# Kernel tuning notes

Measured on AMD Instinct MI355X. Metric: run time of the kernel, lower is better.

Reference implementation:

```python
import jax, jax.numpy as jnp
import numpy as np

B, L, D, DP = 64, 4096, 512, 64


def setup_inputs() -> dict:
    key = jax.random.key(0)
    ks = jax.random.split(key, 7)
    s = 0.02
    return {
        "source": jax.random.normal(ks[0], (B, D), jnp.float32),
        "main_embs": jax.random.normal(ks[1], (L, B, D), jnp.float32),   # time-major memory bank
        "pos_embs": jax.random.normal(ks[2], (L, B, DP), jnp.float32),
        "W_main_in": jax.random.normal(ks[3], (D, D), jnp.float32) * s,  # main_scorer.linear_in (no bias)
        "W_pos_in": jax.random.normal(ks[4], (D, DP), jnp.float32) * s,  # pos_scorer.linear_in (no bias)
        "W_out": jax.random.normal(ks[5], (D, 2 * D), jnp.float32) * s,  # linear_out (no bias, attn_type!='mlp')
        "memory_lengths": jnp.maximum(jax.random.randint(ks[6], (B,), 1, L + 1), 1),
    }


def reference(source, main_embs, pos_embs, W_main_in, W_pos_in, W_out, memory_lengths):
    # to batch-major: (B, L, D) / (B, L, DP)
    me = jnp.transpose(main_embs, (1, 0, 2))
    pe = jnp.transpose(pos_embs, (1, 0, 2))

    # 'general' scorer: project context then dot with query (qrs_len == 1)
    mc = jnp.einsum("bld,ed->ble", me, W_main_in)          # (B, L, D)
    main_align = jnp.einsum("bd,bld->bl", source, mc)      # (B, L)
    pc = jnp.einsum("blp,dp->bld", pe, W_pos_in)           # (B, L, D)
    pos_align = jnp.einsum("bd,bld->bl", source, pc)       # (B, L)

    # length mask + softmax on each branch
    mask = jnp.arange(me.shape[1])[None, :] < memory_lengths[:, None]  # (B, L)
    neg_inf = jnp.float32(-jnp.inf)
    ma = jax.nn.softmax(jnp.where(mask, main_align, neg_inf), axis=-1)
    pa = jax.nn.softmax(jnp.where(mask, pos_align, neg_inf), axis=-1)

    # elementwise combine + renormalize
    av = ma * pa
    av = av / jnp.sum(av, axis=-1, keepdims=True)

    # context vector + output projection + tanh
    c_t = jnp.einsum("bl,bld->bd", av, me)                 # (B, D)
    concat_c = jnp.concatenate([c_t, source], axis=-1)     # (B, 2D)
    attn_h = jnp.tanh(concat_c @ W_out.T)                  # (B, D)

    return attn_h, av, ma, pa
```

## Files before the change

kernel.cpp:

```cpp
#include <hip/hip_runtime.h>
#include <cstddef>

#define NB 64
#define NL 4096
#define ND 512
#define NDP 64
#define LC 64
#define NLC (NL / LC)

__global__ void __launch_bounds__(128) queries_kernel(
    const float* __restrict__ source, const float* __restrict__ Wmi,
    const float* __restrict__ Wpi, float* __restrict__ qpm,
    float* __restrict__ qpp)
{
    __shared__ float s[128];
    const int b  = blockIdx.x >> 2;
    const int eq = blockIdx.x & 3;
    const int t  = threadIdx.x;
    const int e0 = eq * 128;
    s[t] = source[b * ND + e0 + t];
    __syncthreads();

    const int d0 = t * 4;
    float4 a0 = {0,0,0,0}, a1 = {0,0,0,0};
    #pragma unroll 4
    for (int e = 0; e < 128; e += 2) {
        const float4 w0 = *(const float4*)(Wmi + (size_t)(e0 + e) * ND + d0);
        const float4 w1 = *(const float4*)(Wmi + (size_t)(e0 + e + 1) * ND + d0);
        const float x0 = s[e], x1 = s[e + 1];
        a0.x = fmaf(x0, w0.x, a0.x); a0.y = fmaf(x0, w0.y, a0.y);
        a0.z = fmaf(x0, w0.z, a0.z); a0.w = fmaf(x0, w0.w, a0.w);
        a1.x = fmaf(x1, w1.x, a1.x); a1.y = fmaf(x1, w1.y, a1.y);
        a1.z = fmaf(x1, w1.z, a1.z); a1.w = fmaf(x1, w1.w, a1.w);
    }
    a0.x += a1.x; a0.y += a1.y; a0.z += a1.z; a0.w += a1.w;
    *(float4*)(qpm + (size_t)(b * 4 + eq) * ND + d0) = a0;

    if (t < NDP) {
        float c0 = 0.f, c1 = 0.f;
        #pragma unroll 4
        for (int e = 0; e < 128; e += 2) {
            c0 = fmaf(s[e],     Wpi[(size_t)(e0 + e) * NDP + t],     c0);
            c1 = fmaf(s[e + 1], Wpi[(size_t)(e0 + e + 1) * NDP + t], c1);
        }
        qpp[(b * 4 + eq) * NDP + t] = c0 + c1;
    }
}

__global__ void __launch_bounds__(256) pass1_kernel(
    const float* __restrict__ me, const float* __restrict__ pe,
    const float* __restrict__ qpm, const float* __restrict__ qpp,
    const int* __restrict__ mem_len,
    float* __restrict__ a_main, float* __restrict__ a_pos,
    float* __restrict__ Sbuf, float* __restrict__ MZ,
    float* __restrict__ MZa, float* __restrict__ MZp)
{
    const int lane = threadIdx.x & 63;
    const int wid  = threadIdx.x >> 6;
    const int bg   = blockIdx.x & 15;
    const int lc   = blockIdx.x >> 4;
    const int b    = (((bg + (lc >> 4)) & 15) << 2) | wid;

    const int len = mem_len[b];
    const int l0  = lc * LC;
    if (l0 >= len) return;
    const int lend = min(l0 + LC, len);

    float4 q0 = {0,0,0,0}, q1 = {0,0,0,0};
    float qp = 0.f;
    #pragma unroll
    for (int eq = 0; eq < 4; ++eq) {
        const float4* qr = (const float4*)(qpm + (size_t)(b * 4 + eq) * ND);
        const float4 u0 = qr[lane], u1 = qr[64 + lane];
        q0.x += u0.x; q0.y += u0.y; q0.z += u0.z; q0.w += u0.w;
        q1.x += u1.x; q1.y += u1.y; q1.z += u1.z; q1.w += u1.w;
        qp += qpp[(b * 4 + eq) * NDP + lane];
    }

    float m = -1e30f, Z = 0.f;
    float Ma = -1e30f, Za = 0.f, Mp = -1e30f, Zp = 0.f;
    float4 S0 = {0,0,0,0}, S1 = {0,0,0,0};

    for (int l = l0; l < lend; ++l) {
        const size_t r = (size_t)l * NB + b;
        const float4* mrow = (const float4*)(me + r * ND);
        const float4 m0 = mrow[lane];
        const float4 m1 = mrow[64 + lane];

        float accm = m0.x*q0.x + m0.y*q0.y + m0.z*q0.z + m0.w*q0.w
                   + m1.x*q1.x + m1.y*q1.y + m1.z*q1.z + m1.w*q1.w;
        float accp = pe[r * NDP + lane] * qp;
        #pragma unroll
        for (int off = 32; off; off >>= 1) {
            accm += __shfl_xor(accm, off);
            accp += __shfl_xor(accp, off);
        }
        if (lane == 0) {
            a_main[(size_t)b * NL + l] = accm;
            a_pos [(size_t)b * NL + l] = accp;
        }

        const float sv = accm + accp;
        const float mn = fmaxf(m, sv);
        const float sc = __expf(m - mn);
        const float w  = __expf(sv - mn);
        Z = Z * sc + w;
        S0.x = fmaf(S0.x, sc, w * m0.x);  S0.y = fmaf(S0.y, sc, w * m0.y);
        S0.z = fmaf(S0.z, sc, w * m0.z);  S0.w = fmaf(S0.w, sc, w * m0.w);
        S1.x = fmaf(S1.x, sc, w * m1.x);  S1.y = fmaf(S1.y, sc, w * m1.y);
        S1.z = fmaf(S1.z, sc, w * m1.z);  S1.w = fmaf(S1.w, sc, w * m1.w);
        m = mn;

        const float mna = fmaxf(Ma, accm);
        Za = Za * __expf(Ma - mna) + __expf(accm - mna);
        Ma = mna;
        const float mnp = fmaxf(Mp, accp);
        Zp = Zp * __expf(Mp - mnp) + __expf(accp - mnp);
        Mp = mnp;
    }

    float* sp = Sbuf + ((size_t)b * NLC + lc) * ND;
    ((float4*)sp)[lane]      = S0;
    ((float4*)sp)[64 + lane] = S1;
    if (lane == 0) {
        const int idx = b * NLC + lc;
        MZ [2*idx] = m;  MZ [2*idx+1] = Z;
        MZa[2*idx] = Ma; MZa[2*idx+1] = Za;
        MZp[2*idx] = Mp; MZp[2*idx+1] = Zp;
    }
}

__global__ void __launch_bounds__(256) combineA_kernel(
    const float* __restrict__ MZ, const float* __restrict__ MZa,
    const float* __restrict__ MZp, const int* __restrict__ mem_len,
    float* __restrict__ coef, float* __restrict__ stats)
{
    const int lane = threadIdx.x & 63;
    const int b = blockIdx.x * 4 + (threadIdx.x >> 6);
    const int nv = (mem_len[b] + LC - 1) >> 6;
    const bool v = lane < nv;
    const int idx = b * NLC + lane;
    const float m  = v ? MZ [2*idx] : -1e30f;
    const float z  = v ? MZ [2*idx+1] : 0.f;
    const float ma = v ? MZa[2*idx] : -1e30f;
    const float za = v ? MZa[2*idx+1] : 0.f;
    const float mp = v ? MZp[2*idx] : -1e30f;
    const float zp = v ? MZp[2*idx+1] : 0.f;

    float M = m, A = ma, P = mp;
    #pragma unroll
    for (int off = 32; off; off >>= 1) {
        M = fmaxf(M, __shfl_xor(M, off));
        A = fmaxf(A, __shfl_xor(A, off));
        P = fmaxf(P, __shfl_xor(P, off));
    }
    float ez = z * __expf(m - M);
    float ea = za * __expf(ma - A);
    float ep = zp * __expf(mp - P);
    #pragma unroll
    for (int off = 32; off; off >>= 1) {
        ez += __shfl_xor(ez, off);
        ea += __shfl_xor(ea, off);
        ep += __shfl_xor(ep, off);
    }
    const float invZ = 1.f / ez;
    coef[idx] = v ? __expf(m - M) * invZ : 0.f;
    if (lane == 0) {
        stats[b*8+0] = A;  stats[b*8+1] = 1.f / ea;
        stats[b*8+2] = P;  stats[b*8+3] = 1.f / ep;
        stats[b*8+4] = M;  stats[b*8+5] = invZ;
    }
}

__global__ void __launch_bounds__(256) combineBF_kernel(
    const float* __restrict__ Sbuf, const float* __restrict__ coef,
    const float* __restrict__ stats, const int* __restrict__ mem_len,
    float* __restrict__ c_t,
    float* __restrict__ a_main, float* __restrict__ a_pos,
    float* __restrict__ out_av)
{
    if (blockIdx.x < 512) {
        __shared__ float sh[4][64];
        const int b = blockIdx.x >> 3, dseg = blockIdx.x & 7;
        const int dl = threadIdx.x & 63, k = threadIdx.x >> 6;
        const int d = dseg * 64 + dl;
        const int nv = (mem_len[b] + LC - 1) >> 6;
        float acc = 0.f;
        for (int lc = k; lc < nv; lc += 4)
            acc = fmaf(coef[b * NLC + lc],
                       Sbuf[((size_t)b * NLC + lc) * ND + d], acc);
        sh[k][dl] = acc;
        __syncthreads();
        if (threadIdx.x < 64)
            c_t[b * ND + dseg * 64 + threadIdx.x] =
                sh[0][threadIdx.x] + sh[1][threadIdx.x] +
                sh[2][threadIdx.x] + sh[3][threadIdx.x];
    } else {
        const int idx = (blockIdx.x - 512) * 256 + threadIdx.x;
        const int b = idx >> 12;
        const int l = idx & (NL - 1);
        const float* st = stats + b * 8;
        const int len = mem_len[b];
        const float a = a_main[idx];
        const float p = a_pos[idx];
        const bool v = l < len;
        a_main[idx] = v ? __expf(a - st[0]) * st[1] : 0.f;
        a_pos [idx] = v ? __expf(p - st[2]) * st[3] : 0.f;
        out_av[idx] = v ? __expf(a + p - st[4]) * st[5] : 0.f;
    }
}

__global__ void __launch_bounds__(256) out_kernel(
    const float* __restrict__ c_t, const float* __restrict__ source,
    const float* __restrict__ Wout, float* __restrict__ attn_h)
{
    __shared__ float cs[2 * ND];
    const int b = blockIdx.x >> 3;
    const int eg = blockIdx.x & 7;
    const int tid = threadIdx.x;

    for (int d = tid; d < ND; d += 256) {
        cs[d] = c_t[b * ND + d];
        cs[ND + d] = source[b * ND + d];
    }
    __syncthreads();

    const int wid = tid >> 6, lane = tid & 63;
    const float4* csv = (const float4*)cs;
    for (int e = eg * 64 + wid; e < eg * 64 + 64; e += 4) {
        const float4* wrow = (const float4*)(Wout + (size_t)e * 2 * ND);
        float acc = 0.f;
        #pragma unroll
        for (int j = 0; j < 4; ++j) {
            const float4 w = wrow[lane + 64 * j];
            const float4 c = csv[lane + 64 * j];
            acc += w.x * c.x + w.y * c.y + w.z * c.z + w.w * c.w;
        }
        #pragma unroll
        for (int off = 32; off; off >>= 1) acc += __shfl_xor(acc, off);
        if (lane == 0) attn_h[(size_t)b * ND + e] = tanhf(acc);
    }
}

extern "C" void kernel_launch(void* const* d_in, const int* in_sizes, int n_in,
                              void* d_out, int out_size, void* d_ws, size_t ws_size,
                              hipStream_t stream)
{
    const float* source = (const float*)d_in[0];
    const float* me     = (const float*)d_in[1];
    const float* pe     = (const float*)d_in[2];
    const float* Wmi    = (const float*)d_in[3];
    const float* Wpi    = (const float*)d_in[4];
    const float* Wout   = (const float*)d_in[5];
    const int*   lens   = (const int*)d_in[6];

    float* out    = (float*)d_out;
    float* attn_h = out;
    float* av     = attn_h + NB * ND;
    float* ma     = av + NB * NL;
    float* pa     = ma + NB * NL;

    float* ws    = (float*)d_ws;
    float* qpm   = ws;
    float* qpp   = qpm + NB * 4 * ND;
    float* Sbuf  = qpp + NB * 4 * NDP;
    float* MZ    = Sbuf + (size_t)NB * NLC * ND;
    float* MZa   = MZ  + NB * NLC * 2;
    float* MZp   = MZa + NB * NLC * 2;
    float* coef  = MZp + NB * NLC * 2;
    float* c_t   = coef + NB * NLC;
    float* stats = c_t + NB * ND;

    queries_kernel <<<NB * 4, 128, 0, stream>>>(source, Wmi, Wpi, qpm, qpp);
    pass1_kernel   <<<NLC * 16, 256, 0, stream>>>(me, pe, qpm, qpp, lens,
                                                  ma, pa, Sbuf, MZ, MZa, MZp);
    combineA_kernel<<<16, 256, 0, stream>>>(MZ, MZa, MZp, lens, coef, stats);
    combineBF_kernel<<<1536, 256, 0, stream>>>(Sbuf, coef, stats, lens,
                                               c_t, ma, pa, av);
    out_kernel     <<<NB * 8, 256, 0, stream>>>(c_t, source, Wout, attn_h);
}
```

Before: 119.7 us.

## Use persistent atomic work queue in pass1 with 4 waves per chunk

Pass1 becomes a persistent kernel of 1024 blocks that pull (chunk, batch) tasks from a global atomic counter. The four waves of a block now split the 64 rows of a single chunk, each taking every fourth row, instead of each wave handling a different batch row. Each wave also prefetches its next row while computing the current one, and partial softmax states are merged in shared memory before one write per chunk. The aim is to balance work across the skewed memory lengths and raise memory-level parallelism, at the cost of an extra memset, per-task atomics and block syncs.

```diff
diff --git a/kernel.cpp b/kernel.cpp
--- a/kernel.cpp
+++ b/kernel.cpp
@@ -7,6 +7,7 @@
 #define NDP 64
 #define LC 64
 #define NLC (NL / LC)
+#define NTASK (NB * NLC)
 
 __global__ void __launch_bounds__(128) queries_kernel(
     const float* __restrict__ source, const float* __restrict__ Wmi,
@@ -53,80 +54,141 @@
     const int* __restrict__ mem_len,
     float* __restrict__ a_main, float* __restrict__ a_pos,
     float* __restrict__ Sbuf, float* __restrict__ MZ,
-    float* __restrict__ MZa, float* __restrict__ MZp)
-{
-    const int lane = threadIdx.x & 63;
-    const int wid  = threadIdx.x >> 6;
-    const int bg   = blockIdx.x & 15;
-    const int lc   = blockIdx.x >> 4;
-    const int b    = (((bg + (lc >> 4)) & 15) << 2) | wid;
-
-    const int len = mem_len[b];
-    const int l0  = lc * LC;
-    if (l0 >= len) return;
-    const int lend = min(l0 + LC, len);
-
-    float4 q0 = {0,0,0,0}, q1 = {0,0,0,0};
-    float qp = 0.f;
-    #pragma unroll
-    for (int eq = 0; eq < 4; ++eq) {
-        const float4* qr = (const float4*)(qpm + (size_t)(b * 4 + eq) * ND);
-        const float4 u0 = qr[lane], u1 = qr[64 + lane];
-        q0.x += u0.x; q0.y += u0.y; q0.z += u0.z; q0.w += u0.w;
-        q1.x += u1.x; q1.y += u1.y; q1.z += u1.z; q1.w += u1.w;
-        qp += qpp[(b * 4 + eq) * NDP + lane];
-    }
-
-    float m = -1e30f, Z = 0.f;
-    float Ma = -1e30f, Za = 0.f, Mp = -1e30f, Zp = 0.f;
-    float4 S0 = {0,0,0,0}, S1 = {0,0,0,0};
-
-    for (int l = l0; l < lend; ++l) {
-        const size_t r = (size_t)l * NB + b;
-        const float4* mrow = (const float4*)(me + r * ND);
-        const float4 m0 = mrow[lane];
-        const float4 m1 = mrow[64 + lane];
-
-        float accm = m0.x*q0.x + m0.y*q0.y + m0.z*q0.z + m0.w*q0.w
-                   + m1.x*q1.x + m1.y*q1.y + m1.z*q1.z + m1.w*q1.w;
-        float accp = pe[r * NDP + lane] * qp;
+    float* __restrict__ MZa, float* __restrict__ MZp,
+    int* __restrict__ counter)
+{
+    __shared__ float sS[4][ND];
+    __shared__ float sStat[4][6];
+    __shared__ int s_task;
+
+    const int tid  = threadIdx.x;
+    const int lane = tid & 63;
+    const int wid  = tid >> 6;
+
+    for (;;) {
+        __syncthreads();
+        if (tid == 0) s_task = atomicAdd(counter, 1);
+        __syncthreads();
+        const int t = s_task;
+        if (t >= NTASK) return;
+
+        const int lc  = t >> 6;
+        const int b   = t & (NB - 1);
+        const int len = mem_len[b];
+        const int l0  = lc * LC;
+        if (l0 >= len) continue;
+        const int lend = min(l0 + LC, len);
+
+        float4 q0 = {0,0,0,0}, q1 = {0,0,0,0};
+        float qp = 0.f;
         #pragma unroll
-        for (int off = 32; off; off >>= 1) {
-            accm += __shfl_xor(accm, off);
-            accp += __shfl_xor(accp, off);
-        }
+        for (int eq = 0; eq < 4; ++eq) {
+            const float4* qr = (const float4*)(qpm + (size_t)(b * 4 + eq) * ND);
+            const float4 u0 = qr[lane], u1 = qr[64 + lane];
+            q0.x += u0.x; q0.y += u0.y; q0.z += u0.z; q0.w += u0.w;
+            q1.x += u1.x; q1.y += u1.y; q1.z += u1.z; q1.w += u1.w;
+            qp += qpp[(b * 4 + eq) * NDP + lane];
+        }
+
+        float m = -1e30f, Z = 0.f;
+        float Ma = -1e30f, Za = 0.f, Mp = -1e30f, Zp = 0.f;
+        float4 S0 = {0,0,0,0}, S1 = {0,0,0,0};
+
+        int l = l0 + wid;
+        if (l < lend) {
+            const float4* mr = (const float4*)(me + ((size_t)l * NB + b) * ND);
+            float4 c0 = mr[lane];
+            float4 c1 = mr[64 + lane];
+            float  pv = pe[((size_t)l * NB + b) * NDP + lane];
+            for (;;) {
+                const int  ln   = min(l + 4, lend - 1);
+                const bool more = (l + 4) < lend;
+                const float4* nr = (const float4*)(me + ((size_t)ln * NB + b) * ND);
+                const float4 n0 = nr[lane];
+                const float4 n1 = nr[64 + lane];
+                const float  pn = pe[((size_t)ln * NB + b) * NDP + lane];
+
+                float accm = c0.x*q0.x + c0.y*q0.y + c0.z*q0.z + c0.w*q0.w
+                           + c1.x*q1.x + c1.y*q1.y + c1.z*q1.z + c1.w*q1.w;
+                float accp = pv * qp;
+                #pragma unroll
+                for (int off = 32; off; off >>= 1) {
+                    accm += __shfl_xor(accm, off);
+                    accp += __shfl_xor(accp, off);
+                }
+                if (lane == 0) {
+                    a_main[(size_t)b * NL + l] = accm;
+                    a_pos [(size_t)b * NL + l] = accp;
+                }
+
+                const float sv = accm + accp;
+                const float mn = fmaxf(m, sv);
+                const float sc = __expf(m - mn);
+                const float w  = __expf(sv - mn);
+                Z = Z * sc + w;
+                S0.x = fmaf(S0.x, sc, w * c0.x);  S0.y = fmaf(S0.y, sc, w * c0.y);
+                S0.z = fmaf(S0.z, sc, w * c0.z);  S0.w = fmaf(S0.w, sc, w * c0.w);
+                S1.x = fmaf(S1.x, sc, w * c1.x);  S1.y = fmaf(S1.y, sc, w * c1.y);
+                S1.z = fmaf(S1.z, sc, w * c1.z);  S1.w = fmaf(S1.w, sc, w * c1.w);
+                m = mn;
+
+                const float mna = fmaxf(Ma, accm);
+                Za = Za * __expf(Ma - mna) + __expf(accm - mna);
+                Ma = mna;
+                const float mnp = fmaxf(Mp, accp);
+                Zp = Zp * __expf(Mp - mnp) + __expf(accp - mnp);
+                Mp = mnp;
+
+                if (!more) break;
+                c0 = n0; c1 = n1; pv = pn; l += 4;
+            }
+        }
+
+        ((float4*)sS[wid])[lane]      = S0;
+        ((float4*)sS[wid])[64 + lane] = S1;
         if (lane == 0) {
-            a_main[(size_t)b * NL + l] = accm;
-            a_pos [(size_t)b * NL + l] = accp;
-        }
-
-        const float sv = accm + accp;
-        const float mn = fmaxf(m, sv);
-        const float sc = __expf(m - mn);
-        const float w  = __expf(sv - mn);
-        Z = Z * sc + w;
-        S0.x = fmaf(S0.x, sc, w * m0.x);  S0.y = fmaf(S0.y, sc, w * m0.y);
-        S0.z = fmaf(S0.z, sc, w * m0.z);  S0.w = fmaf(S0.w, sc, w * m0.w);
-        S1.x = fmaf(S1.x, sc, w * m1.x);  S1.y = fmaf(S1.y, sc, w * m1.y);
-        S1.z = fmaf(S1.z, sc, w * m1.z);  S1.w = fmaf(S1.w, sc, w * m1.w);
-        m = mn;
-
-        const float mna = fmaxf(Ma, accm);
-        Za = Za * __expf(Ma - mna) + __expf(accm - mna);
-        Ma = mna;
-        const float mnp = fmaxf(Mp, accp);
-        Zp = Zp * __expf(Mp - mnp) + __expf(accp - mnp);
-        Mp = mnp;
-    }
-
-    float* sp = Sbuf + ((size_t)b * NLC + lc) * ND;
-    ((float4*)sp)[lane]      = S0;
-    ((float4*)sp)[64 + lane] = S1;
-    if (lane == 0) {
-        const int idx = b * NLC + lc;
-        MZ [2*idx] = m;  MZ [2*idx+1] = Z;
-        MZa[2*idx] = Ma; MZa[2*idx+1] = Za;
-        MZp[2*idx] = Mp; MZp[2*idx+1] = Zp;
+            sStat[wid][0] = m;  sStat[wid][1] = Z;
+            sStat[wid][2] = Ma; sStat[wid][3] = Za;
+            sStat[wid][4] = Mp; sStat[wid][5] = Zp;
+        }
+        __syncthreads();
+
+        const float w0m = sStat[0][0], w1m = sStat[1][0],
+                    w2m = sStat[2][0], w3m = sStat[3][0];
+        const float mM = fmaxf(fmaxf(w0m, w1m), fmaxf(w2m, w3m));
+        const float e0 = __expf(w0m - mM), e1 = __expf(w1m - mM),
+                    e2 = __expf(w2m - mM), e3 = __expf(w3m - mM);
+        const float2 v0 = ((const float2*)sS[0])[tid];
+        const float2 v1 = ((const float2*)sS[1])[tid];
+        const float2 v2 = ((const float2*)sS[2])[tid];
+        const float2 v3 = ((const float2*)sS[3])[tid];
+        float2 acc;
+        acc.x = v0.x*e0 + v1.x*e1 + v2.x*e2 + v3.x*e3;
+        acc.y = v0.y*e0 + v1.y*e1 + v2.y*e2 + v3.y*e3;
+        ((float2*)(Sbuf + ((size_t)b * NLC + lc) * ND))[tid] = acc;
+
+        if (tid == 0) {
+            const int idx = b * NLC + lc;
+            const float ZM = sStat[0][1]*e0 + sStat[1][1]*e1
+                           + sStat[2][1]*e2 + sStat[3][1]*e3;
+            MZ[2*idx] = mM;  MZ[2*idx+1] = ZM;
+
+            const float A = fmaxf(fmaxf(sStat[0][2], sStat[1][2]),
+                                  fmaxf(sStat[2][2], sStat[3][2]));
+            const float ZA = sStat[0][3]*__expf(sStat[0][2]-A)
+                           + sStat[1][3]*__expf(sStat[1][2]-A)
+                           + sStat[2][3]*__expf(sStat[2][2]-A)
+                           + sStat[3][3]*__expf(sStat[3][2]-A);
+            MZa[2*idx] = A;  MZa[2*idx+1] = ZA;
+
+            const float P = fmaxf(fmaxf(sStat[0][4], sStat[1][4]),
+                                  fmaxf(sStat[2][4], sStat[3][4]));
+            const float ZP = sStat[0][5]*__expf(sStat[0][4]-P)
+                           + sStat[1][5]*__expf(sStat[1][4]-P)
+                           + sStat[2][5]*__expf(sStat[2][4]-P)
+                           + sStat[3][5]*__expf(sStat[3][4]-P);
+            MZp[2*idx] = P;  MZp[2*idx+1] = ZP;
+        }
     }
 }
 
@@ -270,12 +332,14 @@
     float* coef  = MZp + NB * NLC * 2;
     float* c_t   = coef + NB * NLC;
     float* stats = c_t + NB * ND;
-
-    queries_kernel <<<NB * 4, 128, 0, stream>>>(source, Wmi, Wpi, qpm, qpp);
-    pass1_kernel   <<<NLC * 16, 256, 0, stream>>>(me, pe, qpm, qpp, lens,
-                                                  ma, pa, Sbuf, MZ, MZa, MZp);
-    combineA_kernel<<<16, 256, 0, stream>>>(MZ, MZa, MZp, lens, coef, stats);
+    int*   ctr   = (int*)(stats + NB * 8);
+
+    hipMemsetAsync(ctr, 0, sizeof(int), stream);
+    queries_kernel  <<<NB * 4, 128, 0, stream>>>(source, Wmi, Wpi, qpm, qpp);
+    pass1_kernel    <<<1024, 256, 0, stream>>>(me, pe, qpm, qpp, lens,
+                                               ma, pa, Sbuf, MZ, MZa, MZp, ctr);
+    combineA_kernel <<<16, 256, 0, stream>>>(MZ, MZa, MZp, lens, coef, stats);
     combineBF_kernel<<<1536, 256, 0, stream>>>(Sbuf, coef, stats, lens,
                                                c_t, ma, pa, av);
-    out_kernel     <<<NB * 8, 256, 0, stream>>>(c_t, source, Wout, attn_h);
-}
+    out_kernel      <<<NB * 8, 256, 0, stream>>>(c_t, source, Wout, attn_h);
+}
```

Result: slower. 147.5 us (+23.2%).

## Restructure attention pass: per-lane pos scores, prefetched rows, split stats finalize kernel

Applied to the files above, without the earlier changes.

The pass1 kernel now computes the 64 positional scores of a chunk up front, one per lane, instead of reducing one score per row. It prefetches the next memory row while the current one is processed, and uses a branchy online softmax with packed v2f FMAs. It also drops the separate main and positional running max/sum tracking. Those statistics are now computed by a new one-block-per-batch finalize kernel that re-reads the raw scores and also normalizes the outputs and builds the chunk coefficients. The context reduction moves to its own kernel. This is meant to cut shuffle reductions and exp work in the bandwidth-bound main loop, at the cost of an extra pass over the score arrays. The pos-embedding read for lanes beyond the chunk length is unguarded, but it stays in bounds of the buffer.

```diff
diff --git a/kernel.cpp b/kernel.cpp
--- a/kernel.cpp
+++ b/kernel.cpp
@@ -7,6 +7,12 @@
 #define NDP 64
 #define LC 64
 #define NLC (NL / LC)
+
+typedef float v2f __attribute__((ext_vector_type(2)));
+
+__device__ __forceinline__ v2f fma2(v2f a, v2f b, v2f c) {
+    return __builtin_elementwise_fma(a, b, c);
+}
 
 __global__ void __launch_bounds__(128) queries_kernel(
     const float* __restrict__ source, const float* __restrict__ Wmi,
@@ -52,9 +58,9 @@
     const float* __restrict__ qpm, const float* __restrict__ qpp,
     const int* __restrict__ mem_len,
     float* __restrict__ a_main, float* __restrict__ a_pos,
-    float* __restrict__ Sbuf, float* __restrict__ MZ,
-    float* __restrict__ MZa, float* __restrict__ MZp)
-{
+    float* __restrict__ Sbuf, float* __restrict__ MZ)
+{
+    __shared__ __align__(16) float qp_lds[4][NDP];
     const int lane = threadIdx.x & 63;
     const int wid  = threadIdx.x >> 6;
     const int bg   = blockIdx.x & 15;
@@ -64,7 +70,7 @@
     const int len = mem_len[b];
     const int l0  = lc * LC;
     if (l0 >= len) return;
-    const int lend = min(l0 + LC, len);
+    const int nrow = min(LC, len - l0);
 
     float4 q0 = {0,0,0,0}, q1 = {0,0,0,0};
     float qp = 0.f;
@@ -76,138 +82,195 @@
         q1.x += u1.x; q1.y += u1.y; q1.z += u1.z; q1.w += u1.w;
         qp += qpp[(b * 4 + eq) * NDP + lane];
     }
-
-    float m = -1e30f, Z = 0.f;
-    float Ma = -1e30f, Za = 0.f, Mp = -1e30f, Zp = 0.f;
-    float4 S0 = {0,0,0,0}, S1 = {0,0,0,0};
-
-    for (int l = l0; l < lend; ++l) {
-        const size_t r = (size_t)l * NB + b;
-        const float4* mrow = (const float4*)(me + r * ND);
-        const float4 m0 = mrow[lane];
-        const float4 m1 = mrow[64 + lane];
-
-        float accm = m0.x*q0.x + m0.y*q0.y + m0.z*q0.z + m0.w*q0.w
-                   + m1.x*q1.x + m1.y*q1.y + m1.z*q1.z + m1.w*q1.w;
-        float accp = pe[r * NDP + lane] * qp;
-        #pragma unroll
-        for (int off = 32; off; off >>= 1) {
+    qp_lds[wid][lane] = qp;
+
+    float accp = 0.f;
+    {
+        const float4* pr = (const float4*)(pe + ((size_t)(l0 + lane) * NB + b) * NDP);
+        #pragma unroll
+        for (int k = 0; k < 16; ++k) {
+            const float4 pv = pr[k];
+            const float4 qv = *(const float4*)&qp_lds[wid][k * 4];
+            accp = fmaf(pv.x, qv.x, accp);
+            accp = fmaf(pv.y, qv.y, accp);
+            accp = fmaf(pv.z, qv.z, accp);
+            accp = fmaf(pv.w, qv.w, accp);
+        }
+        if (lane < nrow) a_pos[(size_t)b * NL + l0 + lane] = accp;
+    }
+    const int accp_i = __float_as_int(accp);
+
+    const size_t rstride = (size_t)NB * ND;
+    const float* rp = me + ((size_t)l0 * NB + b) * ND;
+    float4 c0 = ((const float4*)rp)[lane];
+    float4 c1 = ((const float4*)rp)[64 + lane];
+
+    float m = -1e30f, Z = 0.f, keep = 0.f;
+    v2f S0 = {0,0}, S1 = {0,0}, S2 = {0,0}, S3 = {0,0};
+
+    for (int i = 0; i < nrow; ++i) {
+        const float* np = rp + ((i + 1 < nrow) ? rstride : 0);
+        const float4 n0 = ((const float4*)np)[lane];
+        const float4 n1 = ((const float4*)np)[64 + lane];
+
+        v2f d2 = {0.f, 0.f};
+        d2 = fma2((v2f){c0.x, c0.y}, (v2f){q0.x, q0.y}, d2);
+        d2 = fma2((v2f){c0.z, c0.w}, (v2f){q0.z, q0.w}, d2);
+        d2 = fma2((v2f){c1.x, c1.y}, (v2f){q1.x, q1.y}, d2);
+        d2 = fma2((v2f){c1.z, c1.w}, (v2f){q1.z, q1.w}, d2);
+        float accm = d2.x + d2.y;
+        #pragma unroll
+        for (int off = 32; off; off >>= 1)
             accm += __shfl_xor(accm, off);
-            accp += __shfl_xor(accp, off);
-        }
-        if (lane == 0) {
-            a_main[(size_t)b * NL + l] = accm;
-            a_pos [(size_t)b * NL + l] = accp;
-        }
-
-        const float sv = accm + accp;
-        const float mn = fmaxf(m, sv);
-        const float sc = __expf(m - mn);
-        const float w  = __expf(sv - mn);
-        Z = Z * sc + w;
-        S0.x = fmaf(S0.x, sc, w * m0.x);  S0.y = fmaf(S0.y, sc, w * m0.y);
-        S0.z = fmaf(S0.z, sc, w * m0.z);  S0.w = fmaf(S0.w, sc, w * m0.w);
-        S1.x = fmaf(S1.x, sc, w * m1.x);  S1.y = fmaf(S1.y, sc, w * m1.y);
-        S1.z = fmaf(S1.z, sc, w * m1.z);  S1.w = fmaf(S1.w, sc, w * m1.w);
-        m = mn;
-
-        const float mna = fmaxf(Ma, accm);
-        Za = Za * __expf(Ma - mna) + __expf(accm - mna);
-        Ma = mna;
-        const float mnp = fmaxf(Mp, accp);
-        Zp = Zp * __expf(Mp - mnp) + __expf(accp - mnp);
-        Mp = mnp;
-    }
+
+        keep = (lane == i) ? accm : keep;
+        const float ap = __int_as_float(__builtin_amdgcn_readlane(accp_i, i));
+        const float sv = accm + ap;
+
+        if (sv > m) {
+            const float sc = __expf(m - sv);
+            const v2f sc2 = {sc, sc};
+            Z = fmaf(Z, sc, 1.f);
+            S0 = fma2(S0, sc2, (v2f){c0.x, c0.y});
+            S1 = fma2(S1, sc2, (v2f){c0.z, c0.w});
+            S2 = fma2(S2, sc2, (v2f){c1.x, c1.y});
+            S3 = fma2(S3, sc2, (v2f){c1.z, c1.w});
+            m = sv;
+        } else {
+            const float w = __expf(sv - m);
+            const v2f w2 = {w, w};
+            Z += w;
+            S0 = fma2((v2f){c0.x, c0.y}, w2, S0);
+            S1 = fma2((v2f){c0.z, c0.w}, w2, S1);
+            S2 = fma2((v2f){c1.x, c1.y}, w2, S2);
+            S3 = fma2((v2f){c1.z, c1.w}, w2, S3);
+        }
+        c0 = n0; c1 = n1;
+        rp += rstride;
+    }
+
+    if (lane < nrow) a_main[(size_t)b * NL + l0 + lane] = keep;
 
     float* sp = Sbuf + ((size_t)b * NLC + lc) * ND;
-    ((float4*)sp)[lane]      = S0;
-    ((float4*)sp)[64 + lane] = S1;
+    ((float4*)sp)[lane]      = (float4){S0.x, S0.y, S1.x, S1.y};
+    ((float4*)sp)[64 + lane] = (float4){S2.x, S2.y, S3.x, S3.y};
     if (lane == 0) {
-        const int idx = b * NLC + lc;
-        MZ [2*idx] = m;  MZ [2*idx+1] = Z;
-        MZa[2*idx] = Ma; MZa[2*idx+1] = Za;
-        MZp[2*idx] = Mp; MZp[2*idx+1] = Zp;
-    }
-}
-
-__global__ void __launch_bounds__(256) combineA_kernel(
-    const float* __restrict__ MZ, const float* __restrict__ MZa,
-    const float* __restrict__ MZp, const int* __restrict__ mem_len,
-    float* __restrict__ coef, float* __restrict__ stats)
-{
-    const int lane = threadIdx.x & 63;
-    const int b = blockIdx.x * 4 + (threadIdx.x >> 6);
+        MZ[2 * (b * NLC + lc)]     = m;
+        MZ[2 * (b * NLC + lc) + 1] = Z;
+    }
+}
+
+__global__ void __launch_bounds__(1024) stats_finalize_kernel(
+    const float* __restrict__ MZ, const int* __restrict__ mem_len,
+    float* __restrict__ ma_io, float* __restrict__ pa_io,
+    float* __restrict__ out_av, float* __restrict__ coef)
+{
+    __shared__ float red[16][6];
+    __shared__ float bc[6];
+    const int b = blockIdx.x;
+    const int tid = threadIdx.x;
+    const int lane = tid & 63, wid = tid >> 6;
+    const int len = mem_len[b];
+
+    float va[4], vp[4];
+    float Am = -1e30f, Pm = -1e30f, Cm = -1e30f;
+    #pragma unroll
+    for (int k = 0; k < 4; ++k) {
+        const int l = tid + k * 1024;
+        va[k] = ma_io[(size_t)b * NL + l];
+        vp[k] = pa_io[(size_t)b * NL + l];
+        if (l < len) {
+            Am = fmaxf(Am, va[k]);
+            Pm = fmaxf(Pm, vp[k]);
+            Cm = fmaxf(Cm, va[k] + vp[k]);
+        }
+    }
+    #pragma unroll
+    for (int off = 32; off; off >>= 1) {
+        Am = fmaxf(Am, __shfl_xor(Am, off));
+        Pm = fmaxf(Pm, __shfl_xor(Pm, off));
+        Cm = fmaxf(Cm, __shfl_xor(Cm, off));
+    }
+    if (lane == 0) { red[wid][0] = Am; red[wid][1] = Pm; red[wid][2] = Cm; }
+    __syncthreads();
+    if (tid < 16) {
+        float a = red[tid][0], p = red[tid][1], c = red[tid][2];
+        #pragma unroll
+        for (int off = 8; off; off >>= 1) {
+            a = fmaxf(a, __shfl_xor(a, off));
+            p = fmaxf(p, __shfl_xor(p, off));
+            c = fmaxf(c, __shfl_xor(c, off));
+        }
+        if (tid == 0) { bc[0] = a; bc[1] = p; bc[2] = c; }
+    }
+    __syncthreads();
+    const float MA = bc[0], MP = bc[1], MC = bc[2];
+
+    float Az = 0.f, Pz = 0.f, Cz = 0.f;
+    #pragma unroll
+    for (int k = 0; k < 4; ++k) {
+        const int l = tid + k * 1024;
+        if (l < len) {
+            Az += __expf(va[k] - MA);
+            Pz += __expf(vp[k] - MP);
+            Cz += __expf(va[k] + vp[k] - MC);
+        }
+    }
+    #pragma unroll
+    for (int off = 32; off; off >>= 1) {
+        Az += __shfl_xor(Az, off);
+        Pz += __shfl_xor(Pz, off);
+        Cz += __shfl_xor(Cz, off);
+    }
+    if (lane == 0) { red[wid][3] = Az; red[wid][4] = Pz; red[wid][5] = Cz; }
+    __syncthreads();
+    if (tid < 16) {
+        float a = red[tid][3], p = red[tid][4], c = red[tid][5];
+        #pragma unroll
+        for (int off = 8; off; off >>= 1) {
+            a += __shfl_xor(a, off);
+            p += __shfl_xor(p, off);
+            c += __shfl_xor(c, off);
+        }
+        if (tid == 0) { bc[3] = a; bc[4] = p; bc[5] = c; }
+    }
+    __syncthreads();
+    const float iA = 1.f / bc[3], iP = 1.f / bc[4], iC = 1.f / bc[5];
+
+    if (tid < NLC) {
+        const int nv = (len + LC - 1) >> 6;
+        const float mlc = MZ[2 * (b * NLC + tid)];
+        coef[b * NLC + tid] = (tid < nv) ? __expf(mlc - MC) * iC : 0.f;
+    }
+
+    #pragma unroll
+    for (int k = 0; k < 4; ++k) {
+        const int l = tid + k * 1024;
+        const bool v = l < len;
+        const size_t idx = (size_t)b * NL + l;
+        ma_io[idx]  = v ? __expf(va[k] - MA) * iA : 0.f;
+        pa_io[idx]  = v ? __expf(vp[k] - MP) * iP : 0.f;
+        out_av[idx] = v ? __expf(va[k] + vp[k] - MC) * iC : 0.f;
+    }
+}
+
+__global__ void __launch_bounds__(256) ctx_kernel(
+    const float* __restrict__ Sbuf, const float* __restrict__ coef,
+    const int* __restrict__ mem_len, float* __restrict__ c_t)
+{
+    __shared__ float sh[3][64];
+    const int b = blockIdx.x >> 3, dseg = blockIdx.x & 7;
+    const int dl = threadIdx.x & 63, k = threadIdx.x >> 6;
+    const int d = dseg * 64 + dl;
     const int nv = (mem_len[b] + LC - 1) >> 6;
-    const bool v = lane < nv;
-    const int idx = b * NLC + lane;
-    const float m  = v ? MZ [2*idx] : -1e30f;
-    const float z  = v ? MZ [2*idx+1] : 0.f;
-    const float ma = v ? MZa[2*idx] : -1e30f;
-    const float za = v ? MZa[2*idx+1] : 0.f;
-    const float mp = v ? MZp[2*idx] : -1e30f;
-    const float zp = v ? MZp[2*idx+1] : 0.f;
-
-    float M = m, A = ma, P = mp;
-    #pragma unroll
-    for (int off = 32; off; off >>= 1) {
-        M = fmaxf(M, __shfl_xor(M, off));
-        A = fmaxf(A, __shfl_xor(A, off));
-        P = fmaxf(P, __shfl_xor(P, off));
-    }
-    float ez = z * __expf(m - M);
-    float ea = za * __expf(ma - A);
-    float ep = zp * __expf(mp - P);
-    #pragma unroll
-    for (int off = 32; off; off >>= 1) {
-        ez += __shfl_xor(ez, off);
-        ea += __shfl_xor(ea, off);
-        ep += __shfl_xor(ep, off);
-    }
-    const float invZ = 1.f / ez;
-    coef[idx] = v ? __expf(m - M) * invZ : 0.f;
-    if (lane == 0) {
-        stats[b*8+0] = A;  stats[b*8+1] = 1.f / ea;
-        stats[b*8+2] = P;  stats[b*8+3] = 1.f / ep;
-        stats[b*8+4] = M;  stats[b*8+5] = invZ;
-    }
-}
-
-__global__ void __launch_bounds__(256) combineBF_kernel(
-    const float* __restrict__ Sbuf, const float* __restrict__ coef,
-    const float* __restrict__ stats, const int* __restrict__ mem_len,
-    float* __restrict__ c_t,
-    float* __restrict__ a_main, float* __restrict__ a_pos,
-    float* __restrict__ out_av)
-{
-    if (blockIdx.x < 512) {
-        __shared__ float sh[4][64];
-        const int b = blockIdx.x >> 3, dseg = blockIdx.x & 7;
-        const int dl = threadIdx.x & 63, k = threadIdx.x >> 6;
-        const int d = dseg * 64 + dl;
-        const int nv = (mem_len[b] + LC - 1) >> 6;
-        float acc = 0.f;
-        for (int lc = k; lc < nv; lc += 4)
-            acc = fmaf(coef[b * NLC + lc],
-                       Sbuf[((size_t)b * NLC + lc) * ND + d], acc);
-        sh[k][dl] = acc;
-        __syncthreads();
-        if (threadIdx.x < 64)
-            c_t[b * ND + dseg * 64 + threadIdx.x] =
-                sh[0][threadIdx.x] + sh[1][threadIdx.x] +
-                sh[2][threadIdx.x] + sh[3][threadIdx.x];
-    } else {
-        const int idx = (blockIdx.x - 512) * 256 + threadIdx.x;
-        const int b = idx >> 12;
-        const int l = idx & (NL - 1);
-        const float* st = stats + b * 8;
-        const int len = mem_len[b];
-        const float a = a_main[idx];
-        const float p = a_pos[idx];
-        const bool v = l < len;
-        a_main[idx] = v ? __expf(a - st[0]) * st[1] : 0.f;
-        a_pos [idx] = v ? __expf(p - st[2]) * st[3] : 0.f;
-        out_av[idx] = v ? __expf(a + p - st[4]) * st[5] : 0.f;
-    }
+    float acc = 0.f;
+    for (int lcc = k; lcc < nv; lcc += 4)
+        acc = fmaf(coef[b * NLC + lcc],
+                   Sbuf[((size_t)b * NLC + lcc) * ND + d], acc);
+    if (k) sh[k - 1][dl] = acc;
+    __syncthreads();
+    if (k == 0)
+        c_t[b * ND + d] = acc + sh[0][dl] + sh[1][dl] + sh[2][dl];
 }
 
 __global__ void __launch_bounds__(256) out_kernel(
@@ -265,17 +328,13 @@
     float* qpp   = qpm + NB * 4 * ND;
     float* Sbuf  = qpp + NB * 4 * NDP;
     float* MZ    = Sbuf + (size_t)NB * NLC * ND;
-    float* MZa   = MZ  + NB * NLC * 2;
-    float* MZp   = MZa + NB * NLC * 2;
-    float* coef  = MZp + NB * NLC * 2;
+    float* coef  = MZ + NB * NLC * 2;
     float* c_t   = coef + NB * NLC;
-    float* stats = c_t + NB * ND;
-
-    queries_kernel <<<NB * 4, 128, 0, stream>>>(source, Wmi, Wpi, qpm, qpp);
-    pass1_kernel   <<<NLC * 16, 256, 0, stream>>>(me, pe, qpm, qpp, lens,
-                                                  ma, pa, Sbuf, MZ, MZa, MZp);
-    combineA_kernel<<<16, 256, 0, stream>>>(MZ, MZa, MZp, lens, coef, stats);
-    combineBF_kernel<<<1536, 256, 0, stream>>>(Sbuf, coef, stats, lens,
-                                               c_t, ma, pa, av);
-    out_kernel     <<<NB * 8, 256, 0, stream>>>(c_t, source, Wout, attn_h);
-}
+
+    queries_kernel        <<<NB * 4, 128, 0, stream>>>(source, Wmi, Wpi, qpm, qpp);
+    pass1_kernel          <<<NLC * 16, 256, 0, stream>>>(me, pe, qpm, qpp, lens,
+                                                         ma, pa, Sbuf, MZ);
+    stats_finalize_kernel <<<NB, 1024, 0, stream>>>(MZ, lens, ma, pa, av, coef);
+    ctx_kernel            <<<NB * 8, 256, 0, stream>>>(Sbuf, coef, lens, c_t);
+    out_kernel            <<<NB * 8, 256, 0, stream>>>(c_t, source, Wout, attn_h);
+}
```

Result: faster. 111.3 us (-7.0%).
